# Kernel tuning notes

Hardware: AMD Instinct MI355X
Metric: run time of the kernel (lower is better)

## Reference

```python
import jax, jax.numpy as jnp
import numpy as np

N_HEAD = 16

def setup_inputs() -> dict:
    key = jax.random.key(0)
    ks = jax.random.split(key, 5)
    C = 1024
    x = jax.random.normal(ks[0], (2, 2048, C), dtype=jnp.float32)
    w_attn = jax.random.normal(ks[1], (C, 3 * C), dtype=jnp.float32) * (C ** -0.5)
    b_attn = jax.random.normal(ks[2], (3 * C,), dtype=jnp.float32) * 0.02
    w_proj = jax.random.normal(ks[3], (C, C), dtype=jnp.float32) * (C ** -0.5)
    b_proj = jax.random.normal(ks[4], (C,), dtype=jnp.float32) * 0.02
    return {"x": x, "w_attn": w_attn, "b_attn": b_attn, "w_proj": w_proj, "b_proj": b_proj}

def reference(x, w_attn, b_attn, w_proj, b_proj):
    B, T, C = x.shape
    H = N_HEAD
    D = C // H  # head_dim
    qkv = x @ w_attn + b_attn  # [B,T,3C]
    q, k, v = jnp.split(qkv, 3, axis=-1)
    # [B,T,H,D] -> [B,H,T,D]
    q = q.reshape(B, T, H, D).transpose(0, 2, 1, 3)
    k = k.reshape(B, T, H, D).transpose(0, 2, 1, 3)
    v = v.reshape(B, T, H, D).transpose(0, 2, 1, 3)
    scale = 1.0 / np.sqrt(D).astype(np.float32)
    att = jnp.einsum('bhqd,bhkd->bhqk', q, k) * scale  # [B,H,T,T]
    causal = jnp.tril(jnp.ones((T, T), dtype=bool))
    att = jnp.where(causal, att, jnp.finfo(att.dtype).min)
    att = jax.nn.softmax(att, axis=-1)
    y = jnp.einsum('bhqk,bhkd->bhqd', att, v)  # [B,H,T,D]
    y = y.transpose(0, 2, 1, 3).reshape(B, T, C)
    return y @ w_proj + b_proj
```

## Files before the change

kernel.cpp:

```cpp
#include <hip/hip_runtime.h>
#include <hip/hip_bf16.h>
#include <stdint.h>

typedef __bf16 bf16x8 __attribute__((ext_vector_type(8)));
typedef __bf16 bf16x4 __attribute__((ext_vector_type(4)));
typedef float  f32x4  __attribute__((ext_vector_type(4)));

#define GLOBAL_AS __attribute__((address_space(1)))
#define LDS_AS    __attribute__((address_space(3)))

__device__ __forceinline__ void gld_lds16(const __bf16* g, __bf16* l) {
  __builtin_amdgcn_global_load_lds((GLOBAL_AS void*)g, (LDS_AS void*)l, 16, 0, 0);
}

#define QSCALE 0.18033688011116029f

__device__ __forceinline__ unsigned pk2(float a, float b) {
  unsigned short ua = __builtin_bit_cast(unsigned short, (__bf16)a);
  unsigned short ub = __builtin_bit_cast(unsigned short, (__bf16)b);
  return (unsigned)ua | ((unsigned)ub << 16);
}

union PackU { unsigned u[4]; bf16x8 v; };

__global__ __launch_bounds__(256) void cast_bf16_kernel(const float* __restrict__ src,
                                                        __bf16* __restrict__ dst, int n)
{
  int i = (blockIdx.x * 256 + threadIdx.x) * 8;
  if (i >= n) return;
  float4 a = *(const float4*)(src + i);
  float4 b = *(const float4*)(src + i + 4);
  bf16x8 o;
  o[0]=(__bf16)a.x; o[1]=(__bf16)a.y; o[2]=(__bf16)a.z; o[3]=(__bf16)a.w;
  o[4]=(__bf16)b.x; o[5]=(__bf16)b.y; o[6]=(__bf16)b.z; o[7]=(__bf16)b.w;
  *(bf16x8*)(dst + i) = o;
}

__global__ __launch_bounds__(256) void transpose_cast_kernel(const float* __restrict__ src,
                                                             __bf16* __restrict__ dst,
                                                             int R, int C)
{
  __shared__ float tile[32][33];
  int c0 = blockIdx.x * 32, r0 = blockIdx.y * 32;
  int tx = threadIdx.x & 31, ty = threadIdx.x >> 5;
  #pragma unroll
  for (int i = 0; i < 32; i += 8)
    tile[ty + i][tx] = src[(size_t)(r0 + ty + i) * C + (c0 + tx)];
  __syncthreads();
  #pragma unroll
  for (int i = 0; i < 32; i += 8)
    dst[(size_t)(c0 + ty + i) * R + (r0 + tx)] = (__bf16)tile[tx][ty + i];
}

template<int MODE>
__global__ __launch_bounds__(256, 2)
void gemm128_kernel(const __bf16* __restrict__ A,
                    const __bf16* __restrict__ Bt,
                    const float*  __restrict__ bias,
                    float* __restrict__ outF,
                    __bf16* __restrict__ qb,
                    __bf16* __restrict__ kb,
                    __bf16* __restrict__ vb,
                    int M, int N, int K)
{
  __shared__ __bf16 As[128 * 32];
  __shared__ __bf16 Bs[128 * 32];
  const int tid  = threadIdx.x;
  const int wave = tid >> 6, lane = tid & 63;
  const int lo = lane & 15, g4 = lane >> 4;
  const int bm = blockIdx.y * 128;
  const int bn = blockIdx.x * 128;
  const int wr = (wave >> 1) * 64;
  const int wc = (wave & 1) * 64;

  f32x4 acc[4][4] = {};

  const int nkt = K >> 5;
  for (int kt = 0; kt < nkt; ++kt) {
    const int k0 = kt << 5;
    __syncthreads();
    #pragma unroll
    for (int j = 0; j < 2; ++j) {
      int c = j * 256 + tid;
      int row = c >> 2, kc = c & 3;
      gld_lds16(A  + (size_t)(bm + row) * K + (k0 + kc * 8), As + c * 8);
      gld_lds16(Bt + (size_t)(bn + row) * K + (k0 + kc * 8), Bs + c * 8);
    }
    __syncthreads();
    bf16x8 af[4], bfr[4];
    #pragma unroll
    for (int mf = 0; mf < 4; ++mf)
      af[mf] = *(const bf16x8*)(As + (wr + mf * 16 + lo) * 32 + g4 * 8);
    #pragma unroll
    for (int nf = 0; nf < 4; ++nf)
      bfr[nf] = *(const bf16x8*)(Bs + (wc + nf * 16 + lo) * 32 + g4 * 8);
    #pragma unroll
    for (int mf = 0; mf < 4; ++mf)
      #pragma unroll
      for (int nf = 0; nf < 4; ++nf)
        acc[mf][nf] = __builtin_amdgcn_mfma_f32_16x16x32_bf16(af[mf], bfr[nf], acc[mf][nf], 0, 0, 0);
  }

  float bv[4];
  #pragma unroll
  for (int nf = 0; nf < 4; ++nf) bv[nf] = bias[bn + wc + nf * 16 + lo];

  if (MODE == 1) {
    #pragma unroll
    for (int mf = 0; mf < 4; ++mf)
      #pragma unroll
      for (int nf = 0; nf < 4; ++nf) {
        int col = bn + wc + nf * 16 + lo;
        #pragma unroll
        for (int j = 0; j < 4; ++j) {
          int row = bm + wr + mf * 16 + g4 * 4 + j;
          outF[(size_t)row * N + col] = acc[mf][nf][j] + bv[nf];
        }
      }
  } else {
    #pragma unroll
    for (int mf = 0; mf < 4; ++mf) {
      const int tbase = bm + wr + mf * 16 + g4 * 4;
      const int b = tbase >> 11, t = tbase & 2047;
      #pragma unroll
      for (int nf = 0; nf < 4; ++nf) {
        int n = bn + wc + nf * 16 + lo;
        int sel = n >> 10, hd = n & 1023;
        int h = hd >> 6, d = hd & 63;
        size_t bh = (size_t)(b * 16 + h);
        if (sel == 2) {
          bf16x4 pv;
          #pragma unroll
          for (int j = 0; j < 4; ++j) pv[j] = (__bf16)(acc[mf][nf][j] + bv[nf]);
          *(bf16x4*)(vb + (bh * 64 + d) * 2048 + t) = pv;
        } else if (sel == 0) {
          #pragma unroll
          for (int j = 0; j < 4; ++j)
            qb[(bh * 2048 + (size_t)(t + j)) * 64 + d] = (__bf16)((acc[mf][nf][j] + bv[nf]) * QSCALE);
        } else {
          #pragma unroll
          for (int j = 0; j < 4; ++j)
            kb[(bh * 2048 + (size_t)(t + j)) * 64 + d] = (__bf16)(acc[mf][nf][j] + bv[nf]);
        }
      }
    }
  }
}

__global__ __launch_bounds__(256, 4)
void attn_kernel(const __bf16* __restrict__ qg, const __bf16* __restrict__ kg,
                 const __bf16* __restrict__ vg, __bf16* __restrict__ yg)
{
  const int idx = blockIdx.x;
  const int hi2 = idx >> 8;
  const int low = idx & 255;
  const int bh  = low & 31;
  const int q8  = low >> 5;
  int strip;
  if      (hi2 == 0) strip = q8;
  else if (hi2 == 1) strip = 31 - q8;
  else if (hi2 == 2) strip = q8 + 8;
  else               strip = 23 - q8;

  const int b = bh >> 4, h = bh & 15;
  const int tid  = threadIdx.x;
  const int wave = tid >> 6;
  const int lane = tid & 63;
  const int l15  = lane & 15;
  const int g    = lane >> 4;

  __shared__ __bf16 Kb[2][64 * 64];
  __shared__ __bf16 Vb[2][64 * 64];

  const __bf16* qbase = qg + (size_t)bh * 2048 * 64;
  const __bf16* kbase = kg + (size_t)bh * 2048 * 64;
  const __bf16* vbase = vg + (size_t)bh * 64 * 2048;

  const int q16 = strip * 64 + wave * 16 + l15;
  bf16x8 qf0 = *(const bf16x8*)(qbase + (size_t)q16 * 64 + g * 8);
  bf16x8 qf1 = *(const bf16x8*)(qbase + (size_t)q16 * 64 + 32 + g * 8);

  f32x4 o0 = {}, o1 = {}, o2 = {}, o3 = {};
  float m_ = -3.0e38f, l_ = 0.f;

  auto STAGE = [&](int t, int bsel) {
    #pragma unroll
    for (int j = 0; j < 2; ++j) {
      int c = j * 256 + tid;
      int r = c >> 3, cc = c & 7;
      int cs = cc ^ (r & 7);
      int pr = (r & 0x23) | ((r & 0x10) >> 2) | ((r & 0x0C) << 1);
      gld_lds16(kbase + (size_t)(t * 64 + pr) * 64 + cs * 8, &Kb[bsel][0] + c * 8);
      gld_lds16(vbase + (size_t)r * 2048 + (t * 64 + cs * 8), &Vb[bsel][0] + c * 8);
    }
  };

  STAGE(0, 0);
  int cur = 0;
  const int niter = strip + 1;
  const int sw = l15 & 7;

  for (int i = 0; i < niter; ++i) {
    __syncthreads();
    if (i + 1 < niter) STAGE(i + 1, cur ^ 1);

    const __bf16* KL = &Kb[cur][0];
    f32x4 s0 = {}, s1 = {}, s2 = {}, s3 = {};
    {
      bf16x8 k00 = *(const bf16x8*)(KL + (0  + l15) * 64 + ((0 + g) ^ sw) * 8);
      bf16x8 k01 = *(const bf16x8*)(KL + (0  + l15) * 64 + ((4 + g) ^ sw) * 8);
      s0 = __builtin_amdgcn_mfma_f32_16x16x32_bf16(k00, qf0, s0, 0, 0, 0);
      s0 = __builtin_amdgcn_mfma_f32_16x16x32_bf16(k01, qf1, s0, 0, 0, 0);
      bf16x8 k10 = *(const bf16x8*)(KL + (16 + l15) * 64 + ((0 + g) ^ sw) * 8);
      bf16x8 k11 = *(const bf16x8*)(KL + (16 + l15) * 64 + ((4 + g) ^ sw) * 8);
      s1 = __builtin_amdgcn_mfma_f32_16x16x32_bf16(k10, qf0, s1, 0, 0, 0);
      s1 = __builtin_amdgcn_mfma_f32_16x16x32_bf16(k11, qf1, s1, 0, 0, 0);
      bf16x8 k20 = *(const bf16x8*)(KL + (32 + l15) * 64 + ((0 + g) ^ sw) * 8);
      bf16x8 k21 = *(const bf16x8*)(KL + (32 + l15) * 64 + ((4 + g) ^ sw) * 8);
      s2 = __builtin_amdgcn_mfma_f32_16x16x32_bf16(k20, qf0, s2, 0, 0, 0);
      s2 = __builtin_amdgcn_mfma_f32_16x16x32_bf16(k21, qf1, s2, 0, 0, 0);
      bf16x8 k30 = *(const bf16x8*)(KL + (48 + l15) * 64 + ((0 + g) ^ sw) * 8);
      bf16x8 k31 = *(const bf16x8*)(KL + (48 + l15) * 64 + ((4 + g) ^ sw) * 8);
      s3 = __builtin_amdgcn_mfma_f32_16x16x32_bf16(k30, qf0, s3, 0, 0, 0);
      s3 = __builtin_amdgcn_mfma_f32_16x16x32_bf16(k31, qf1, s3, 0, 0, 0);
    }

    if (i == strip) {
      const int qr = wave * 16 + l15;
      #pragma unroll
      for (int r = 0; r < 4; ++r) {
        if (8 * g + r          > qr) s0[r] = -3.0e38f;
        if (8 * g + 4 + r      > qr) s1[r] = -3.0e38f;
        if (32 + 8 * g + r     > qr) s2[r] = -3.0e38f;
        if (32 + 8 * g + 4 + r > qr) s3[r] = -3.0e38f;
      }
    }

    float h0 = fmaxf(fmaxf(s0[0], s0[1]), fmaxf(s0[2], s0[3]));
    float h1 = fmaxf(fmaxf(s1[0], s1[1]), fmaxf(s1[2], s1[3]));
    float h2 = fmaxf(fmaxf(s2[0], s2[1]), fmaxf(s2[2], s2[3]));
    float h3 = fmaxf(fmaxf(s3[0], s3[1]), fmaxf(s3[2], s3[3]));
    float pm = fmaxf(fmaxf(h0, h1), fmaxf(h2, h3));
    pm = fmaxf(pm, __shfl_xor(pm, 16, 64));
    pm = fmaxf(pm, __shfl_xor(pm, 32, 64));

    if (__any(pm > m_ + 8.f)) {
      float mnew = fmaxf(m_, pm);
      float alpha = exp2f(m_ - mnew);
      m_ = mnew;
      l_ *= alpha;
      float a0 = __shfl(alpha, 4 * g + 0, 64);
      float a1 = __shfl(alpha, 4 * g + 1, 64);
      float a2 = __shfl(alpha, 4 * g + 2, 64);
      float a3 = __shfl(alpha, 4 * g + 3, 64);
      o0[0] *= a0; o0[1] *= a1; o0[2] *= a2; o0[3] *= a3;
      o1[0] *= a0; o1[1] *= a1; o1[2] *= a2; o1[3] *= a3;
      o2[0] *= a0; o2[1] *= a1; o2[2] *= a2; o2[3] *= a3;
      o3[0] *= a0; o3[1] *= a1; o3[2] *= a2; o3[3] *= a3;
    }

    float rs = 0.f;
    #pragma unroll
    for (int r = 0; r < 4; ++r) { s0[r] = exp2f(s0[r] - m_); rs += s0[r]; }
    #pragma unroll
    for (int r = 0; r < 4; ++r) { s1[r] = exp2f(s1[r] - m_); rs += s1[r]; }
    #pragma unroll
    for (int r = 0; r < 4; ++r) { s2[r] = exp2f(s2[r] - m_); rs += s2[r]; }
    #pragma unroll
    for (int r = 0; r < 4; ++r) { s3[r] = exp2f(s3[r] - m_); rs += s3[r]; }
    rs += __shfl_xor(rs, 16, 64);
    rs += __shfl_xor(rs, 32, 64);
    l_ += rs;

    PackU pa0, pa1;
    pa0.u[0] = pk2(s0[0], s0[1]); pa0.u[1] = pk2(s0[2], s0[3]);
    pa0.u[2] = pk2(s1[0], s1[1]); pa0.u[3] = pk2(s1[2], s1[3]);
    pa1.u[0] = pk2(s2[0], s2[1]); pa1.u[1] = pk2(s2[2], s2[3]);
    pa1.u[2] = pk2(s3[0], s3[1]); pa1.u[3] = pk2(s3[2], s3[3]);

    const __bf16* VL = &Vb[cur][0];
    {
      bf16x8 v00 = *(const bf16x8*)(VL + (0  + l15) * 64 + ((0 + g) ^ sw) * 8);
      bf16x8 v01 = *(const bf16x8*)(VL + (0  + l15) * 64 + ((4 + g) ^ sw) * 8);
      o0 = __builtin_amdgcn_mfma_f32_16x16x32_bf16(pa0.v, v00, o0, 0, 0, 0);
      o0 = __builtin_amdgcn_mfma_f32_16x16x32_bf16(pa1.v, v01, o0, 0, 0, 0);
      bf16x8 v10 = *(const bf16x8*)(VL + (16 + l15) * 64 + ((0 + g) ^ sw) * 8);
      bf16x8 v11 = *(const bf16x8*)(VL + (16 + l15) * 64 + ((4 + g) ^ sw) * 8);
      o1 = __builtin_amdgcn_mfma_f32_16x16x32_bf16(pa0.v, v10, o1, 0, 0, 0);
      o1 = __builtin_amdgcn_mfma_f32_16x16x32_bf16(pa1.v, v11, o1, 0, 0, 0);
      bf16x8 v20 = *(const bf16x8*)(VL + (32 + l15) * 64 + ((0 + g) ^ sw) * 8);
      bf16x8 v21 = *(const bf16x8*)(VL + (32 + l15) * 64 + ((4 + g) ^ sw) * 8);
      o2 = __builtin_amdgcn_mfma_f32_16x16x32_bf16(pa0.v, v20, o2, 0, 0, 0);
      o2 = __builtin_amdgcn_mfma_f32_16x16x32_bf16(pa1.v, v21, o2, 0, 0, 0);
      bf16x8 v30 = *(const bf16x8*)(VL + (48 + l15) * 64 + ((0 + g) ^ sw) * 8);
      bf16x8 v31 = *(const bf16x8*)(VL + (48 + l15) * 64 + ((4 + g) ^ sw) * 8);
      o3 = __builtin_amdgcn_mfma_f32_16x16x32_bf16(pa0.v, v30, o3, 0, 0, 0);
      o3 = __builtin_amdgcn_mfma_f32_16x16x32_bf16(pa1.v, v31, o3, 0, 0, 0);
    }

    cur ^= 1;
  }

  float invl = 1.0f / l_;
  #pragma unroll
  for (int r = 0; r < 4; ++r) {
    float il = __shfl(invl, 4 * g + r, 64);
    int trow = strip * 64 + wave * 16 + 4 * g + r;
    __bf16* dst = yg + ((size_t)(b * 2048 + trow)) * 1024 + h * 64;
    dst[l15]      = (__bf16)(o0[r] * il);
    dst[16 + l15] = (__bf16)(o1[r] * il);
    dst[32 + l15] = (__bf16)(o2[r] * il);
    dst[48 + l15] = (__bf16)(o3[r] * il);
  }
}

extern "C" void kernel_launch(void* const* d_in, const int* in_sizes, int n_in,
                              void* d_out, int out_size, void* d_ws, size_t ws_size,
                              hipStream_t stream)
{
  const float* x      = (const float*)d_in[0];
  const float* w_attn = (const float*)d_in[1];
  const float* b_attn = (const float*)d_in[2];
  const float* w_proj = (const float*)d_in[3];
  const float* b_proj = (const float*)d_in[4];
  float* out = (float*)d_out;

  __bf16* xb  = (__bf16*)d_ws;
  __bf16* waT = xb  + (size_t)4096 * 1024;
  __bf16* wpT = waT + (size_t)3072 * 1024;
  __bf16* qb  = wpT + (size_t)1024 * 1024;
  __bf16* kb  = qb  + (size_t)32 * 2048 * 64;
  __bf16* vb  = kb  + (size_t)32 * 2048 * 64;
  __bf16* yb  = vb  + (size_t)32 * 2048 * 64;

  cast_bf16_kernel<<<2048, 256, 0, stream>>>(x, xb, 4096 * 1024);
  transpose_cast_kernel<<<dim3(96, 32), 256, 0, stream>>>(w_attn, waT, 1024, 3072);
  transpose_cast_kernel<<<dim3(32, 32), 256, 0, stream>>>(w_proj, wpT, 1024, 1024);
  gemm128_kernel<0><<<dim3(24, 32), 256, 0, stream>>>(xb, waT, b_attn, nullptr,
                                                      qb, kb, vb, 4096, 3072, 1024);
  attn_kernel<<<1024, 256, 0, stream>>>(qb, kb, vb, yb);
  gemm128_kernel<1><<<dim3(8, 32), 256, 0, stream>>>(yb, wpT, b_proj, out,
                                                     nullptr, nullptr, nullptr, 4096, 1024, 1024);
}
```

Measured before the change: 116.1 us.

## Balance causal attention work with split-KV partials and merge kernel

Replaces the strip-pairing block order with a scheme where every block does about 17 KV tiles. Blocks with t<16 finish query strip t, then process part of long strip 31-t. Blocks with t>=16 handle the first 16 tiles of strip t. The two partial results for the long strips are combined in a new merge kernel using saved row max and row sum values. The row sum is now computed with an MFMA against a ones vector instead of shuffles. This adds an extra launch, partial-output traffic, bf16 rounding of the partials, and reuse of workspace buffers for them.

Measured after the change: 122.0 us. +5.0%, slower.

```diff
diff --git a/kernel.cpp b/kernel.cpp
--- a/kernel.cpp
+++ b/kernel.cpp
@@ -149,25 +149,20 @@
 
 __global__ __launch_bounds__(256, 4)
 void attn_kernel(const __bf16* __restrict__ qg, const __bf16* __restrict__ kg,
-                 const __bf16* __restrict__ vg, __bf16* __restrict__ yg)
+                 const __bf16* __restrict__ vg, __bf16* __restrict__ yg,
+                 __bf16* __restrict__ pY, float* __restrict__ pM, float* __restrict__ pL)
 {
   const int idx = blockIdx.x;
-  const int hi2 = idx >> 8;
-  const int low = idx & 255;
-  const int bh  = low & 31;
-  const int q8  = low >> 5;
-  int strip;
-  if      (hi2 == 0) strip = q8;
-  else if (hi2 == 1) strip = 31 - q8;
-  else if (hi2 == 2) strip = q8 + 8;
-  else               strip = 23 - q8;
-
+  const int bh  = idx >> 5;
+  const int t   = idx & 31;
   const int b = bh >> 4, h = bh & 15;
+
   const int tid  = threadIdx.x;
   const int wave = tid >> 6;
   const int lane = tid & 63;
   const int l15  = lane & 15;
   const int g    = lane >> 4;
+  const int sw   = l15 & 7;
 
   __shared__ __bf16 Kb[2][64 * 64];
   __shared__ __bf16 Vb[2][64 * 64];
@@ -176,34 +171,36 @@
   const __bf16* kbase = kg + (size_t)bh * 2048 * 64;
   const __bf16* vbase = vg + (size_t)bh * 64 * 2048;
 
-  const int q16 = strip * 64 + wave * 16 + l15;
-  bf16x8 qf0 = *(const bf16x8*)(qbase + (size_t)q16 * 64 + g * 8);
-  bf16x8 qf1 = *(const bf16x8*)(qbase + (size_t)q16 * 64 + 32 + g * 8);
-
-  f32x4 o0 = {}, o1 = {}, o2 = {}, o3 = {};
-  float m_ = -3.0e38f, l_ = 0.f;
-
-  auto STAGE = [&](int t, int bsel) {
+  bf16x8 qf0, qf1;
+  f32x4 o0, o1, o2, o3, osum;
+  float m_;
+
+  bf16x8 ones;
+  #pragma unroll
+  for (int j = 0; j < 8; ++j) ones[j] = (__bf16)1.0f;
+
+  auto LOADQ = [&](int strip) {
+    const int q16 = strip * 64 + wave * 16 + l15;
+    qf0 = *(const bf16x8*)(qbase + (size_t)q16 * 64 + g * 8);
+    qf1 = *(const bf16x8*)(qbase + (size_t)q16 * 64 + 32 + g * 8);
+  };
+  auto RESET = [&]() {
+    o0 = f32x4{}; o1 = f32x4{}; o2 = f32x4{}; o3 = f32x4{}; osum = f32x4{};
+    m_ = -3.0e38f;
+  };
+  auto STAGE = [&](int kt, int bsel) {
     #pragma unroll
     for (int j = 0; j < 2; ++j) {
       int c = j * 256 + tid;
       int r = c >> 3, cc = c & 7;
       int cs = cc ^ (r & 7);
       int pr = (r & 0x23) | ((r & 0x10) >> 2) | ((r & 0x0C) << 1);
-      gld_lds16(kbase + (size_t)(t * 64 + pr) * 64 + cs * 8, &Kb[bsel][0] + c * 8);
-      gld_lds16(vbase + (size_t)r * 2048 + (t * 64 + cs * 8), &Vb[bsel][0] + c * 8);
-    }
-  };
-
-  STAGE(0, 0);
-  int cur = 0;
-  const int niter = strip + 1;
-  const int sw = l15 & 7;
-
-  for (int i = 0; i < niter; ++i) {
-    __syncthreads();
-    if (i + 1 < niter) STAGE(i + 1, cur ^ 1);
-
+      gld_lds16(kbase + (size_t)(kt * 64 + pr) * 64 + cs * 8, &Kb[bsel][0] + c * 8);
+      gld_lds16(vbase + (size_t)r * 2048 + (kt * 64 + cs * 8), &Vb[bsel][0] + c * 8);
+    }
+  };
+
+  auto TILE = [&](int cur, bool diag) {
     const __bf16* KL = &Kb[cur][0];
     f32x4 s0 = {}, s1 = {}, s2 = {}, s3 = {};
     {
@@ -225,7 +222,7 @@
       s3 = __builtin_amdgcn_mfma_f32_16x16x32_bf16(k31, qf1, s3, 0, 0, 0);
     }
 
-    if (i == strip) {
+    if (diag) {
       const int qr = wave * 16 + l15;
       #pragma unroll
       for (int r = 0; r < 4; ++r) {
@@ -248,7 +245,6 @@
       float mnew = fmaxf(m_, pm);
       float alpha = exp2f(m_ - mnew);
       m_ = mnew;
-      l_ *= alpha;
       float a0 = __shfl(alpha, 4 * g + 0, 64);
       float a1 = __shfl(alpha, 4 * g + 1, 64);
       float a2 = __shfl(alpha, 4 * g + 2, 64);
@@ -257,26 +253,26 @@
       o1[0] *= a0; o1[1] *= a1; o1[2] *= a2; o1[3] *= a3;
       o2[0] *= a0; o2[1] *= a1; o2[2] *= a2; o2[3] *= a3;
       o3[0] *= a0; o3[1] *= a1; o3[2] *= a2; o3[3] *= a3;
-    }
-
-    float rs = 0.f;
-    #pragma unroll
-    for (int r = 0; r < 4; ++r) { s0[r] = exp2f(s0[r] - m_); rs += s0[r]; }
-    #pragma unroll
-    for (int r = 0; r < 4; ++r) { s1[r] = exp2f(s1[r] - m_); rs += s1[r]; }
-    #pragma unroll
-    for (int r = 0; r < 4; ++r) { s2[r] = exp2f(s2[r] - m_); rs += s2[r]; }
-    #pragma unroll
-    for (int r = 0; r < 4; ++r) { s3[r] = exp2f(s3[r] - m_); rs += s3[r]; }
-    rs += __shfl_xor(rs, 16, 64);
-    rs += __shfl_xor(rs, 32, 64);
-    l_ += rs;
+      osum[0] *= a0; osum[1] *= a1; osum[2] *= a2; osum[3] *= a3;
+    }
+
+    #pragma unroll
+    for (int r = 0; r < 4; ++r) s0[r] = exp2f(s0[r] - m_);
+    #pragma unroll
+    for (int r = 0; r < 4; ++r) s1[r] = exp2f(s1[r] - m_);
+    #pragma unroll
+    for (int r = 0; r < 4; ++r) s2[r] = exp2f(s2[r] - m_);
+    #pragma unroll
+    for (int r = 0; r < 4; ++r) s3[r] = exp2f(s3[r] - m_);
 
     PackU pa0, pa1;
     pa0.u[0] = pk2(s0[0], s0[1]); pa0.u[1] = pk2(s0[2], s0[3]);
     pa0.u[2] = pk2(s1[0], s1[1]); pa0.u[3] = pk2(s1[2], s1[3]);
     pa1.u[0] = pk2(s2[0], s2[1]); pa1.u[1] = pk2(s2[2], s2[3]);
     pa1.u[2] = pk2(s3[0], s3[1]); pa1.u[3] = pk2(s3[2], s3[3]);
+
+    osum = __builtin_amdgcn_mfma_f32_16x16x32_bf16(pa0.v, ones, osum, 0, 0, 0);
+    osum = __builtin_amdgcn_mfma_f32_16x16x32_bf16(pa1.v, ones, osum, 0, 0, 0);
 
     const __bf16* VL = &Vb[cur][0];
     {
@@ -297,21 +293,103 @@
       o3 = __builtin_amdgcn_mfma_f32_16x16x32_bf16(pa0.v, v30, o3, 0, 0, 0);
       o3 = __builtin_amdgcn_mfma_f32_16x16x32_bf16(pa1.v, v31, o3, 0, 0, 0);
     }
-
-    cur ^= 1;
+  };
+
+  auto WRITE_Y = [&](int strip) {
+    #pragma unroll
+    for (int r = 0; r < 4; ++r) {
+      float il = 1.0f / osum[r];
+      int trow = strip * 64 + wave * 16 + 4 * g + r;
+      __bf16* dst = yg + ((size_t)(b * 2048 + trow)) * 1024 + h * 64;
+      dst[l15]      = (__bf16)(o0[r] * il);
+      dst[16 + l15] = (__bf16)(o1[r] * il);
+      dst[32 + l15] = (__bf16)(o2[r] * il);
+      dst[48 + l15] = (__bf16)(o3[r] * il);
+    }
+  };
+  auto WRITE_PART = [&](int slot) {
+    #pragma unroll
+    for (int r = 0; r < 4; ++r) {
+      float il = 1.0f / osum[r];
+      int row = wave * 16 + 4 * g + r;
+      __bf16* dst = pY + (size_t)slot * 4096 + row * 64;
+      dst[l15]      = (__bf16)(o0[r] * il);
+      dst[16 + l15] = (__bf16)(o1[r] * il);
+      dst[32 + l15] = (__bf16)(o2[r] * il);
+      dst[48 + l15] = (__bf16)(o3[r] * il);
+    }
+    if (g == 0) pM[slot * 64 + wave * 16 + l15] = m_;
+    if (l15 == 0) {
+      #pragma unroll
+      for (int r = 0; r < 4; ++r) pL[slot * 64 + wave * 16 + 4 * g + r] = osum[r];
+    }
+  };
+
+  int cur = 0;
+  if (t < 16) {
+    LOADQ(t); RESET();
+    STAGE(0, 0);
+    for (int i = 0; i <= t; ++i) {
+      __syncthreads();
+      int nx = i + 1;
+      STAGE((nx <= t) ? nx : (nx + 15 - t), cur ^ 1);
+      TILE(cur, i == t);
+      cur ^= 1;
+    }
+    WRITE_Y(t);
+    LOADQ(31 - t); RESET();
+    for (int i = t + 1; i <= 16; ++i) {
+      __syncthreads();
+      if (i < 16) STAGE(i + 16 - t, cur ^ 1);
+      TILE(cur, i == 16);
+      cur ^= 1;
+    }
+    WRITE_PART((bh * 16 + 15 - t) * 2 + 1);
+  } else {
+    LOADQ(t); RESET();
+    STAGE(0, 0);
+    for (int i = 0; i < 16; ++i) {
+      __syncthreads();
+      if (i < 15) STAGE(i + 1, cur ^ 1);
+      TILE(cur, false);
+      cur ^= 1;
+    }
+    WRITE_PART((bh * 16 + (t - 16)) * 2);
   }
-
-  float invl = 1.0f / l_;
+}
+
+__global__ __launch_bounds__(256)
+void attn_merge_kernel(const __bf16* __restrict__ pY, const float* __restrict__ pM,
+                       const float* __restrict__ pL, __bf16* __restrict__ yg)
+{
+  const int us = blockIdx.x & 15, bh = blockIdx.x >> 4;
+  const int b = bh >> 4, h = bh & 15;
+  const int tid = threadIdx.x;
+  const int row = tid >> 2, d0 = (tid & 3) * 16;
+  const int slotA = (bh * 16 + us) * 2, slotB = slotA + 1;
+
+  float mA = pM[slotA * 64 + row], lA = pL[slotA * 64 + row];
+  float mB = pM[slotB * 64 + row], lB = pL[slotB * 64 + row];
+  float mx = fmaxf(mA, mB);
+  float wA = exp2f(mA - mx) * lA;
+  float wB = exp2f(mB - mx) * lB;
+  float inv = 1.0f / (wA + wB);
+  wA *= inv; wB *= inv;
+
+  const __bf16* ya = pY + (size_t)slotA * 4096 + row * 64 + d0;
+  const __bf16* yb = pY + (size_t)slotB * 4096 + row * 64 + d0;
+  __bf16* dst = yg + ((size_t)(b * 2048 + (16 + us) * 64 + row)) * 1024 + h * 64 + d0;
+
+  bf16x8 a0 = *(const bf16x8*)ya, a1 = *(const bf16x8*)(ya + 8);
+  bf16x8 b0 = *(const bf16x8*)yb, b1 = *(const bf16x8*)(yb + 8);
+  bf16x8 r0, r1;
   #pragma unroll
-  for (int r = 0; r < 4; ++r) {
-    float il = __shfl(invl, 4 * g + r, 64);
-    int trow = strip * 64 + wave * 16 + 4 * g + r;
-    __bf16* dst = yg + ((size_t)(b * 2048 + trow)) * 1024 + h * 64;
-    dst[l15]      = (__bf16)(o0[r] * il);
-    dst[16 + l15] = (__bf16)(o1[r] * il);
-    dst[32 + l15] = (__bf16)(o2[r] * il);
-    dst[48 + l15] = (__bf16)(o3[r] * il);
+  for (int j = 0; j < 8; ++j) {
+    r0[j] = (__bf16)(wA * (float)a0[j] + wB * (float)b0[j]);
+    r1[j] = (__bf16)(wA * (float)a1[j] + wB * (float)b1[j]);
   }
+  *(bf16x8*)dst = r0;
+  *(bf16x8*)(dst + 8) = r1;
 }
 
 extern "C" void kernel_launch(void* const* d_in, const int* in_sizes, int n_in,
@@ -333,12 +411,17 @@
   __bf16* vb  = kb  + (size_t)32 * 2048 * 64;
   __bf16* yb  = vb  + (size_t)32 * 2048 * 64;
 
+  __bf16* pY = xb;
+  float*  pM = (float*)waT;
+  float*  pL = pM + 1024 * 64;
+
   cast_bf16_kernel<<<2048, 256, 0, stream>>>(x, xb, 4096 * 1024);
   transpose_cast_kernel<<<dim3(96, 32), 256, 0, stream>>>(w_attn, waT, 1024, 3072);
   transpose_cast_kernel<<<dim3(32, 32), 256, 0, stream>>>(w_proj, wpT, 1024, 1024);
   gemm128_kernel<0><<<dim3(24, 32), 256, 0, stream>>>(xb, waT, b_attn, nullptr,
                                                       qb, kb, vb, 4096, 3072, 1024);
-  attn_kernel<<<1024, 256, 0, stream>>>(qb, kb, vb, yb);
+  attn_kernel<<<1024, 256, 0, stream>>>(qb, kb, vb, yb, pY, pM, pL);
+  attn_merge_kernel<<<512, 256, 0, stream>>>(pY, pM, pL, yb);
   gemm128_kernel<1><<<dim3(8, 32), 256, 0, stream>>>(yb, wpT, b_proj, out,
                                                      nullptr, nullptr, nullptr, 4096, 1024, 1024);
 }
```
